# Performance work log

Hardware: AMD Instinct MI355X
Metric: run time of the kernel (lower is better)

Reference implementation:

```python
import jax, jax.numpy as jnp
import numpy as np

BATCH = 128
N = 4000
N_A = 400
STEPNUM = 100


def f_real(u):
    # 0.5*u*(3-u^2) + (300/12)*u^2*(3/4 - 2u + 3/2 u^2 - 1/4 u^4)
    return 0.5 * u * (3.0 - u ** 2) + 25.0 * u ** 2 * (0.75 - 2.0 * u + 1.5 * u ** 2 - 0.25 * u ** 4)


# elementwise df/du (f_real is elementwise, so grad of the sum gives per-element derivative)
_f_prime = jax.grad(lambda v: jnp.sum(f_real(v)))


def a_real(u):
    return jnp.where(u < 0.5, 0.0, 1.0).astype(u.dtype)


def setup_inputs() -> dict:
    key = jax.random.key(0)
    init = jax.random.uniform(key, (BATCH, N), dtype=jnp.float32)  # u in [0,1]
    u_a = jnp.tile(jnp.linspace(0.0, 1.0, N_A + 1, dtype=jnp.float32)[None, :], (BATCH, 1))
    dt = jnp.array([4e-6], dtype=jnp.float32)
    dx = jnp.array([10.0 / N], dtype=jnp.float32)
    return {"init": init, "u_a": u_a, "dt": dt, "dx": dx, "stepnum": STEPNUM}


def _forward(init, u_a, dt, dx, stepnum):
    dt = dt[0]
    dx = dx[0]
    # a = 0.5 * a_real(u_a); cumulative trapezoid A_a[:, j] = trapz(a[:, :j+1], u_a[:, :j+1])
    a = 0.5 * a_real(u_a)
    seg = 0.5 * (a[:, 1:] + a[:, :-1]) * (u_a[:, 1:] - u_a[:, :-1])
    A_a = jnp.concatenate([jnp.zeros_like(a[:, :1]), jnp.cumsum(seg, axis=1)], axis=1)  # (B, N_a+1)
    interp = jax.vmap(jnp.interp)  # per-batch-row 1d linear interpolation (Interp1d)

    def step(u_old, _):
        f = f_real(u_old)                                   # (B, N)
        # df/du computed on a detached copy (b = u.clone().detach()) -> stop_gradient
        dfdu = jnp.abs(_f_prime(jax.lax.stop_gradient(u_old)))
        M = jnp.maximum(dfdu[:, :-1], dfdu[:, 1:])          # (B, N-1)
        f_half = 0.5 * (f[:, :-1] + f[:, 1:]) - 0.5 * M * (u_old[:, 1:] - u_old[:, :-1])
        A_u = interp(u_old, u_a, A_a)                       # A(u) lookup, (B, N)
        A_half = (A_u[:, 1:] - A_u[:, :-1]) / dx            # (B, N-1)
        interior = (u_old[:, 1:-1]
                    - dt / dx * (f_half[:, 1:] - f_half[:, :-1])
                    + dt / dx * (A_half[:, 1:] - A_half[:, :-1]))
        # boundary: u[:,0] = u[:,1]; u[:,N-1] = u[:,N-2]
        u = jnp.concatenate([interior[:, :1], interior, interior[:, -1:]], axis=1)
        return u, u

    _, traj = jax.lax.scan(step, init, None, length=stepnum)
    return jnp.concatenate([init[None], traj], axis=0)  # (stepnum+1, B, N)


def reference(init, u_a, dt, dx, stepnum):
    return _forward(init, u_a, dt, dx, stepnum)
```

## Files before the change

kernel.cpp:

```cpp
#include <hip/hip_runtime.h>

#define BATCH  128
#define NPTS   4000
#define NA     400
#define BN     (BATCH * NPTS)

#define CHUNKS 4
#define CHUNK  (NPTS / CHUNKS)
#define SSTEPS 50
#define HALO   52
#define LLEN   (CHUNK + 2 * HALO)
#define NACT   (LLEN / 4)
#define TPB    320

__device__ __forceinline__ float f_real(float u) {
    float u2 = u * u;
    float p  = fmaf(u2, fmaf(u2, -0.25f, 1.5f), fmaf(u, -2.0f, 0.75f));
    return u * fmaf(u2, -0.5f, 1.5f) + 25.0f * u2 * p;
}

__device__ __forceinline__ float fprime(float u) {
    float u2 = u * u;
    return fmaf(u, fmaf(u, fmaf(u, fmaf(u2, -37.5f, 150.0f), -151.5f), 37.5f), 1.5f);
}

__device__ __forceinline__ float A_of_u(float u, float xlo, float xhi,
                                        float Aj0, float Amax) {
    float m = fmaxf(0.25f * (u - xlo), fmaf(0.5f, u - xhi, Aj0));
    m = fmaxf(m, 0.0f);
    return fminf(m, Amax);
}

__device__ __forceinline__ int iclamp(int v, int lo, int hi) {
    return v < lo ? lo : (v > hi ? hi : v);
}

__global__ __launch_bounds__(TPB)
void vclin_step_kernel(const float* __restrict__ src,
                       float* __restrict__ out,
                       const float* __restrict__ u_a,
                       const float* __restrict__ dtp,
                       const float* __restrict__ dxp,
                       int step0, int write_src) {
    __shared__ float hL[2][TPB];
    __shared__ float hR[2][TPB];
    __shared__ float tbl[3];

    const int t     = threadIdx.x;
    const int row   = blockIdx.x >> 2;
    const int chunk = blockIdx.x & 3;
    const int own_start = chunk * CHUNK;
    const int ls    = own_start - HALO;
    const int gbase = ls + 4 * t;
    const bool active = (t < NACT);
    const bool owner  = active && gbase >= own_start && gbase < own_start + CHUNK;
    const size_t rowbase = (size_t)row * NPTS;

    const float* ua_row = u_a + (size_t)row * (NA + 1);
    for (int k = t + 1; k <= NA; k += TPB) {
        float a = ua_row[k - 1], b = ua_row[k];
        if (a < 0.5f && b >= 0.5f) { tbl[0] = a; tbl[1] = b; tbl[2] = ua_row[NA]; }
    }

    const float DT  = dtp[0];
    const float DX  = dxp[0];
    const float lam = DT / DX;
    const float invdx = 1.0f / DX;

    float u0 = 0.f, u1 = 0.f, u2 = 0.f, u3 = 0.f;
    if (active) {
        if (gbase >= 0 && gbase + 3 < NPTS) {
            float4 v = *reinterpret_cast<const float4*>(src + rowbase + gbase);
            u0 = v.x; u1 = v.y; u2 = v.z; u3 = v.w;
        } else {
            u0 = src[rowbase + iclamp(gbase,     0, NPTS - 1)];
            u1 = src[rowbase + iclamp(gbase + 1, 0, NPTS - 1)];
            u2 = src[rowbase + iclamp(gbase + 2, 0, NPTS - 1)];
            u3 = src[rowbase + iclamp(gbase + 3, 0, NPTS - 1)];
        }
    }

    __syncthreads();
    const float xlo  = tbl[0];
    const float xhi  = tbl[1];
    const float Aj0  = 0.25f * (xhi - xlo);
    const float Amax = fmaf(0.5f, tbl[2] - xhi, Aj0);

    float* wp = nullptr;
    if (owner) {
        wp = out + (size_t)(step0 + 1) * BN + rowbase + gbase;
        if (write_src) {
            float4 v; v.x = u0; v.y = u1; v.z = u2; v.w = u3;
            *reinterpret_cast<float4*>(out + rowbase + gbase) = v;
        }
    }

    for (int s = 0; s < SSTEPS; ++s) {
        const int p = s & 1;
        float f0, f1, f2, f3, g0, g1, g2, g3, A0, A1, A2, A3;
        if (active) {
            hL[p][t] = u0; hR[p][t] = u3;
            f0 = f_real(u0); f1 = f_real(u1); f2 = f_real(u2); f3 = f_real(u3);
            g0 = fabsf(fprime(u0)); g1 = fabsf(fprime(u1));
            g2 = fabsf(fprime(u2)); g3 = fabsf(fprime(u3));
            A0 = A_of_u(u0, xlo, xhi, Aj0, Amax);
            A1 = A_of_u(u1, xlo, xhi, Aj0, Amax);
            A2 = A_of_u(u2, xlo, xhi, Aj0, Amax);
            A3 = A_of_u(u3, xlo, xhi, Aj0, Amax);
        }
        __syncthreads();
        if (active) {
            float lu = (t > 0)        ? hR[p][t - 1] : u0;
            float ru = (t < NACT - 1) ? hL[p][t + 1] : u3;
            float lf = f_real(lu), lg = fabsf(fprime(lu));
            float la = A_of_u(lu, xlo, xhi, Aj0, Amax);
            float rf = f_real(ru), rg = fabsf(fprime(ru));
            float ra = A_of_u(ru, xlo, xhi, Aj0, Amax);

            float F0 = 0.5f * (lf + f0) - 0.5f * fmaxf(lg, g0) * (u0 - lu) - invdx * (A0 - la);
            float F1 = 0.5f * (f0 + f1) - 0.5f * fmaxf(g0, g1) * (u1 - u0) - invdx * (A1 - A0);
            float F2 = 0.5f * (f1 + f2) - 0.5f * fmaxf(g1, g2) * (u2 - u1) - invdx * (A2 - A1);
            float F3 = 0.5f * (f2 + f3) - 0.5f * fmaxf(g2, g3) * (u3 - u2) - invdx * (A3 - A2);
            float F4 = 0.5f * (f3 + rf) - 0.5f * fmaxf(g3, rg) * (ru - u3) - invdx * (ra - A3);

            float nu0 = fmaf(-lam, F1 - F0, u0);
            float nu1 = fmaf(-lam, F2 - F1, u1);
            float nu2 = fmaf(-lam, F3 - F2, u2);
            float nu3 = fmaf(-lam, F4 - F3, u3);

            if (gbase == 0)        nu0 = nu1;
            if (gbase == NPTS - 4) nu3 = nu2;

            u0 = nu0; u1 = nu1; u2 = nu2; u3 = nu3;
            if (owner) {
                float4 v; v.x = u0; v.y = u1; v.z = u2; v.w = u3;
                *reinterpret_cast<float4*>(wp) = v;
                wp += BN;
            }
        }
    }
}

extern "C" void kernel_launch(void* const* d_in, const int* in_sizes, int n_in,
                              void* d_out, int out_size, void* d_ws, size_t ws_size,
                              hipStream_t stream) {
    const float* init = (const float*)d_in[0];
    const float* u_a  = (const float*)d_in[1];
    const float* dt   = (const float*)d_in[2];
    const float* dx   = (const float*)d_in[3];
    float* out = (float*)d_out;

    const int grid = BATCH * CHUNKS;

    hipLaunchKernelGGL(vclin_step_kernel, dim3(grid), dim3(TPB), 0, stream,
                       init, out, u_a, dt, dx, 0, 1);
    hipLaunchKernelGGL(vclin_step_kernel, dim3(grid), dim3(TPB), 0, stream,
                       out + (size_t)SSTEPS * BN, out, u_a, dt, dx, SSTEPS, 0);
}
```

Measured before the change: 281.4 us.

## Replace block-level LDS halo exchange with single-wavefront shuffle stencil

Each block becomes one 64-lane wavefront handling 8 cells per lane over a 512-point window (400 owned plus 56-point halos), exchanging neighbour values with shuffles instead of shared memory and per-step __syncthreads. The row is split into 10 chunks instead of 4, giving more blocks. The u_a breakpoint search is done with a ballot/shuffle instead of shared memory. This removes barrier and LDS overhead per step at the cost of more redundant halo computation.

```diff
diff --git a/kernel.cpp b/kernel.cpp
--- a/kernel.cpp
+++ b/kernel.cpp
@@ -5,13 +5,11 @@
 #define NA     400
 #define BN     (BATCH * NPTS)
 
-#define CHUNKS 4
-#define CHUNK  (NPTS / CHUNKS)
+#define CHUNKS 10
+#define OWN    (NPTS / CHUNKS)
+#define HALO   56
+#define CPL    8
 #define SSTEPS 50
-#define HALO   52
-#define LLEN   (CHUNK + 2 * HALO)
-#define NACT   (LLEN / 4)
-#define TPB    320
 
 __device__ __forceinline__ float f_real(float u) {
     float u2 = u * u;
@@ -19,124 +17,133 @@
     return u * fmaf(u2, -0.5f, 1.5f) + 25.0f * u2 * p;
 }
 
-__device__ __forceinline__ float fprime(float u) {
+__device__ __forceinline__ float fprime_abs(float u) {
     float u2 = u * u;
-    return fmaf(u, fmaf(u, fmaf(u, fmaf(u2, -37.5f, 150.0f), -151.5f), 37.5f), 1.5f);
+    return fabsf(fmaf(u, fmaf(u, fmaf(u, fmaf(u2, -37.5f, 150.0f), -151.5f), 37.5f), 1.5f));
 }
 
 __device__ __forceinline__ float A_of_u(float u, float xlo, float xhi,
                                         float Aj0, float Amax) {
     float m = fmaxf(0.25f * (u - xlo), fmaf(0.5f, u - xhi, Aj0));
-    m = fmaxf(m, 0.0f);
-    return fminf(m, Amax);
+    return fminf(fmaxf(m, 0.0f), Amax);
 }
 
 __device__ __forceinline__ int iclamp(int v, int lo, int hi) {
     return v < lo ? lo : (v > hi ? hi : v);
 }
 
-__global__ __launch_bounds__(TPB)
-void vclin_step_kernel(const float* __restrict__ src,
+__global__ __launch_bounds__(64)
+void vclin_wave_kernel(const float* __restrict__ src,
                        float* __restrict__ out,
                        const float* __restrict__ u_a,
                        const float* __restrict__ dtp,
                        const float* __restrict__ dxp,
                        int step0, int write_src) {
-    __shared__ float hL[2][TPB];
-    __shared__ float hR[2][TPB];
-    __shared__ float tbl[3];
-
-    const int t     = threadIdx.x;
-    const int row   = blockIdx.x >> 2;
-    const int chunk = blockIdx.x & 3;
-    const int own_start = chunk * CHUNK;
-    const int ls    = own_start - HALO;
-    const int gbase = ls + 4 * t;
-    const bool active = (t < NACT);
-    const bool owner  = active && gbase >= own_start && gbase < own_start + CHUNK;
+    const int lane  = threadIdx.x;
+    const int w     = blockIdx.x;
+    const int row   = w / CHUNKS;
+    const int chunk = w - row * CHUNKS;
+    const int own_start = chunk * OWN;
+    const int gbase = own_start - HALO + CPL * lane;
+    const bool owner = (gbase >= own_start) && (gbase < own_start + OWN);
     const size_t rowbase = (size_t)row * NPTS;
 
     const float* ua_row = u_a + (size_t)row * (NA + 1);
-    for (int k = t + 1; k <= NA; k += TPB) {
-        float a = ua_row[k - 1], b = ua_row[k];
-        if (a < 0.5f && b >= 0.5f) { tbl[0] = a; tbl[1] = b; tbl[2] = ua_row[NA]; }
+    float xlo = 0.0f, xhi = 1.0f;
+    bool found = false;
+    #pragma unroll
+    for (int j = 0; j < 7; ++j) {
+        int k = 7 * lane + j;
+        if (k < NA) {
+            float a = ua_row[k], b = ua_row[k + 1];
+            if (a < 0.5f && b >= 0.5f) { xlo = a; xhi = b; found = true; }
+        }
     }
+    unsigned long long m = __ballot(found);
+    int srcLane = (m != 0ull) ? (__ffsll((long long)m) - 1) : 0;
+    xlo = __shfl(xlo, srcLane);
+    xhi = __shfl(xhi, srcLane);
+    const float xmax = ua_row[NA];
+    const float Aj0  = 0.25f * (xhi - xlo);
+    const float Amax = fmaf(0.5f, xmax - xhi, Aj0);
 
     const float DT  = dtp[0];
     const float DX  = dxp[0];
     const float lam = DT / DX;
     const float invdx = 1.0f / DX;
 
-    float u0 = 0.f, u1 = 0.f, u2 = 0.f, u3 = 0.f;
-    if (active) {
-        if (gbase >= 0 && gbase + 3 < NPTS) {
-            float4 v = *reinterpret_cast<const float4*>(src + rowbase + gbase);
-            u0 = v.x; u1 = v.y; u2 = v.z; u3 = v.w;
-        } else {
-            u0 = src[rowbase + iclamp(gbase,     0, NPTS - 1)];
-            u1 = src[rowbase + iclamp(gbase + 1, 0, NPTS - 1)];
-            u2 = src[rowbase + iclamp(gbase + 2, 0, NPTS - 1)];
-            u3 = src[rowbase + iclamp(gbase + 3, 0, NPTS - 1)];
-        }
+    float u[CPL];
+    if (gbase >= 0 && gbase + CPL <= NPTS) {
+        float4 a = *reinterpret_cast<const float4*>(src + rowbase + gbase);
+        float4 b = *reinterpret_cast<const float4*>(src + rowbase + gbase + 4);
+        u[0] = a.x; u[1] = a.y; u[2] = a.z; u[3] = a.w;
+        u[4] = b.x; u[5] = b.y; u[6] = b.z; u[7] = b.w;
+    } else {
+        #pragma unroll
+        for (int c = 0; c < CPL; ++c)
+            u[c] = src[rowbase + iclamp(gbase + c, 0, NPTS - 1)];
     }
-
-    __syncthreads();
-    const float xlo  = tbl[0];
-    const float xhi  = tbl[1];
-    const float Aj0  = 0.25f * (xhi - xlo);
-    const float Amax = fmaf(0.5f, tbl[2] - xhi, Aj0);
 
     float* wp = nullptr;
     if (owner) {
         wp = out + (size_t)(step0 + 1) * BN + rowbase + gbase;
         if (write_src) {
-            float4 v; v.x = u0; v.y = u1; v.z = u2; v.w = u3;
-            *reinterpret_cast<float4*>(out + rowbase + gbase) = v;
+            float4 a; a.x = u[0]; a.y = u[1]; a.z = u[2]; a.w = u[3];
+            float4 b; b.x = u[4]; b.y = u[5]; b.z = u[6]; b.w = u[7];
+            *reinterpret_cast<float4*>(out + rowbase + gbase)     = a;
+            *reinterpret_cast<float4*>(out + rowbase + gbase + 4) = b;
         }
     }
 
+    const bool bcL = (gbase == 0);
+    const bool bcR = (gbase == NPTS - CPL);
+
     for (int s = 0; s < SSTEPS; ++s) {
-        const int p = s & 1;
-        float f0, f1, f2, f3, g0, g1, g2, g3, A0, A1, A2, A3;
-        if (active) {
-            hL[p][t] = u0; hR[p][t] = u3;
-            f0 = f_real(u0); f1 = f_real(u1); f2 = f_real(u2); f3 = f_real(u3);
-            g0 = fabsf(fprime(u0)); g1 = fabsf(fprime(u1));
-            g2 = fabsf(fprime(u2)); g3 = fabsf(fprime(u3));
-            A0 = A_of_u(u0, xlo, xhi, Aj0, Amax);
-            A1 = A_of_u(u1, xlo, xhi, Aj0, Amax);
-            A2 = A_of_u(u2, xlo, xhi, Aj0, Amax);
-            A3 = A_of_u(u3, xlo, xhi, Aj0, Amax);
+        float f[CPL], g[CPL], A[CPL];
+        #pragma unroll
+        for (int c = 0; c < CPL; ++c) {
+            f[c] = f_real(u[c]);
+            g[c] = fprime_abs(u[c]);
+            A[c] = A_of_u(u[c], xlo, xhi, Aj0, Amax);
         }
-        __syncthreads();
-        if (active) {
-            float lu = (t > 0)        ? hR[p][t - 1] : u0;
-            float ru = (t < NACT - 1) ? hL[p][t + 1] : u3;
-            float lf = f_real(lu), lg = fabsf(fprime(lu));
-            float la = A_of_u(lu, xlo, xhi, Aj0, Amax);
-            float rf = f_real(ru), rg = fabsf(fprime(ru));
-            float ra = A_of_u(ru, xlo, xhi, Aj0, Amax);
 
-            float F0 = 0.5f * (lf + f0) - 0.5f * fmaxf(lg, g0) * (u0 - lu) - invdx * (A0 - la);
-            float F1 = 0.5f * (f0 + f1) - 0.5f * fmaxf(g0, g1) * (u1 - u0) - invdx * (A1 - A0);
-            float F2 = 0.5f * (f1 + f2) - 0.5f * fmaxf(g1, g2) * (u2 - u1) - invdx * (A2 - A1);
-            float F3 = 0.5f * (f2 + f3) - 0.5f * fmaxf(g2, g3) * (u3 - u2) - invdx * (A3 - A2);
-            float F4 = 0.5f * (f3 + rf) - 0.5f * fmaxf(g3, rg) * (ru - u3) - invdx * (ra - A3);
+        float lu = __shfl_up(u[CPL - 1], 1);
+        float lf = __shfl_up(f[CPL - 1], 1);
+        float lg = __shfl_up(g[CPL - 1], 1);
+        float lA = __shfl_up(A[CPL - 1], 1);
+        float ru = __shfl_down(u[0], 1);
+        float rf = __shfl_down(f[0], 1);
+        float rg = __shfl_down(g[0], 1);
+        float rA = __shfl_down(A[0], 1);
+        if (lane == 0)  { lu = u[0]; lf = f[0]; lg = g[0]; lA = A[0]; }
+        if (lane == 63) { ru = u[CPL-1]; rf = f[CPL-1]; rg = g[CPL-1]; rA = A[CPL-1]; }
 
-            float nu0 = fmaf(-lam, F1 - F0, u0);
-            float nu1 = fmaf(-lam, F2 - F1, u1);
-            float nu2 = fmaf(-lam, F3 - F2, u2);
-            float nu3 = fmaf(-lam, F4 - F3, u3);
+        float F[CPL + 1];
+        F[0] = 0.5f * (lf + f[0]) - 0.5f * fmaxf(lg, g[0]) * (u[0] - lu) - invdx * (A[0] - lA);
+        #pragma unroll
+        for (int c = 1; c < CPL; ++c)
+            F[c] = 0.5f * (f[c-1] + f[c]) - 0.5f * fmaxf(g[c-1], g[c]) * (u[c] - u[c-1])
+                 - invdx * (A[c] - A[c-1]);
+        F[CPL] = 0.5f * (f[CPL-1] + rf) - 0.5f * fmaxf(g[CPL-1], rg) * (ru - u[CPL-1])
+               - invdx * (rA - A[CPL-1]);
 
-            if (gbase == 0)        nu0 = nu1;
-            if (gbase == NPTS - 4) nu3 = nu2;
+        float nu[CPL];
+        #pragma unroll
+        for (int c = 0; c < CPL; ++c)
+            nu[c] = fmaf(-lam, F[c + 1] - F[c], u[c]);
 
-            u0 = nu0; u1 = nu1; u2 = nu2; u3 = nu3;
-            if (owner) {
-                float4 v; v.x = u0; v.y = u1; v.z = u2; v.w = u3;
-                *reinterpret_cast<float4*>(wp) = v;
-                wp += BN;
-            }
+        if (bcL) nu[0] = nu[1];
+        if (bcR) nu[CPL - 1] = nu[CPL - 2];
+
+        #pragma unroll
+        for (int c = 0; c < CPL; ++c) u[c] = nu[c];
+
+        if (owner) {
+            float4 a; a.x = u[0]; a.y = u[1]; a.z = u[2]; a.w = u[3];
+            float4 b; b.x = u[4]; b.y = u[5]; b.z = u[6]; b.w = u[7];
+            *reinterpret_cast<float4*>(wp)     = a;
+            *reinterpret_cast<float4*>(wp + 4) = b;
+            wp += BN;
         }
     }
 }
@@ -152,8 +159,8 @@
 
     const int grid = BATCH * CHUNKS;
 
-    hipLaunchKernelGGL(vclin_step_kernel, dim3(grid), dim3(TPB), 0, stream,
+    hipLaunchKernelGGL(vclin_wave_kernel, dim3(grid), dim3(64), 0, stream,
                        init, out, u_a, dt, dx, 0, 1);
-    hipLaunchKernelGGL(vclin_step_kernel, dim3(grid), dim3(TPB), 0, stream,
+    hipLaunchKernelGGL(vclin_wave_kernel, dim3(grid), dim3(64), 0, stream,
                        out + (size_t)SSTEPS * BN, out, u_a, dt, dx, SSTEPS, 0);
 }
```

New measurement: 264.7 us. 1.06x faster.
